# Performance work log

Hardware: AMD Instinct MI355X
Metric: run time of the kernel (lower is better)

Reference implementation:

```python
import jax, jax.numpy as jnp
import numpy as np

B, T, W, E, H, EMB, NVOCAB, WIN = 256, 200, 200, 768, 256, 32, 201, 8


def setup_inputs() -> dict:
    key = jax.random.key(0)
    ks = jax.random.split(key, 12)
    s = 0.05
    inputs = jax.random.normal(ks[0], (B, T, E), jnp.float32)
    full_word_embeddings = jax.random.normal(ks[1], (B, W, E), jnp.float32)
    lengths = jax.random.randint(ks[2], (B,), T // 2, T + 1)
    fix = jax.random.randint(ks[3], (B, T), 1, NVOCAB)
    fix_seq = jnp.where(jnp.arange(T)[None, :] < lengths[:, None], fix, 0)
    emb_table = (jax.random.normal(ks[4], (NVOCAB, EMB)) * s).at[0].set(0.0)  # padding_idx=0
    W_ih = jax.random.normal(ks[5], (3 * H, E + EMB)) * s  # torch GRU layout, gates r,z,n
    W_hh = jax.random.normal(ks[6], (3 * H, H)) * s
    b_ih = jax.random.normal(ks[7], (3 * H,)) * s
    b_hh = jax.random.normal(ks[8], (3 * H,)) * s
    W_out = jax.random.normal(ks[9], (E, H)) * s  # output_layer: Linear(H, E)
    b_out = jnp.zeros((E,), jnp.float32)
    W_dur = jax.random.normal(ks[10], (1, H)) * s  # duration_layer: Linear(H, 1)
    b_dur = jnp.zeros((1,), jnp.float32)
    return {"inputs": inputs, "fix_seq": fix_seq, "full_word_embeddings": full_word_embeddings,
            "lengths": lengths, "expert_id": 0, "emb_table": emb_table,
            "W_ih": W_ih, "b_ih": b_ih, "W_hh": W_hh, "b_hh": b_hh,
            "W_out": W_out, "b_out": b_out, "W_dur": W_dur, "b_dur": b_dur}


def _gru(x, W_ih, b_ih, W_hh, b_hh, h_dim):
    # x: [B,T,I]. Precompute input projections once, scan over time.
    xg = jnp.einsum('bti,gi->btg', x, W_ih) + b_ih  # [B,T,3H]

    def step(h, xg_t):
        hg = h @ W_hh.T + b_hh
        xr, xz, xn = jnp.split(xg_t, 3, axis=-1)
        hr, hz, hn = jnp.split(hg, 3, axis=-1)
        r = jax.nn.sigmoid(xr + hr)
        z = jax.nn.sigmoid(xz + hz)
        n = jnp.tanh(xn + r * hn)
        h_new = (1.0 - z) * n + z * h
        return h_new, h_new

    h0 = jnp.zeros((x.shape[0], h_dim), x.dtype)
    _, outs = jax.lax.scan(step, h0, jnp.swapaxes(xg, 0, 1))
    return jnp.swapaxes(outs, 0, 1)  # [B,T,H]


def reference(inputs, fix_seq, full_word_embeddings, lengths, expert_id,
              emb_table, W_ih, b_ih, W_hh, b_hh, W_out, b_out, W_dur, b_dur):
    del expert_id  # weights of the selected expert are passed directly
    valid_mask = fix_seq != 0
    scan_emb = emb_table[fix_seq]  # [B,T,32]
    rnn_in = jnp.concatenate([inputs, scan_emb], axis=-1)
    outputs = _gru(rnn_in, W_ih, b_ih, W_hh, b_hh, W_hh.shape[1])  # [B,T,H]
    # pad_packed_sequence zeros outputs beyond each sequence length
    tmask = jnp.arange(outputs.shape[1])[None, :] < lengths[:, None]
    outputs = outputs * tmask[..., None].astype(outputs.dtype)
    # dot attention: proj then scores against word embeddings
    proj = outputs @ W_out.T + b_out  # [B,T,E]
    logits = jnp.einsum('bte,bwe->btw', proj, full_word_embeddings)
    # saccade window mask around current fixation position
    wpos = jnp.arange(full_word_embeddings.shape[1])[None, None, :]
    dist = jnp.abs(wpos - fix_seq[..., None])
    sacc = (dist <= WIN) & valid_mask[..., None]
    logits = jnp.where(sacc, logits, -1e9)
    word_mask = jnp.sum(jnp.abs(full_word_embeddings), axis=-1) != 0
    logits = jnp.where(word_mask[:, None, :], logits, -1e9)
    dur_pred = (outputs @ W_dur.T + b_dur)[..., 0]  # [B,T]
    return logits, dur_pred
```

## Files before the change

kernel.cpp:

```cpp
#include <hip/hip_runtime.h>
#include <hip/hip_bf16.h>

typedef __attribute__((ext_vector_type(8))) short bf16x8;
typedef __attribute__((ext_vector_type(4))) float f32x4;
typedef __attribute__((ext_vector_type(4))) int   i32x4;

#define NB 256
#define NT 200
#define NW 200
#define NE 768
#define NH 256
#define NEMB 32
#define KIN 800
#define G3H 768
#define MROWS 51200

__device__ __forceinline__ float bf2f(unsigned short h) {
    return __uint_as_float(((unsigned)h) << 16);
}
__device__ __forceinline__ unsigned short f2bf(float f) {
    unsigned u = __float_as_uint(f);
    u += 0x7fff + ((u >> 16) & 1);
    return (unsigned short)(u >> 16);
}
__device__ __forceinline__ float sigm(float x) { return 1.0f / (1.0f + __expf(-x)); }
__device__ __forceinline__ float tanh_fast(float x) {
    float e = __expf(2.0f * x);
    return 1.0f - 2.0f / (e + 1.0f);
}

#if __has_builtin(__builtin_amdgcn_sdot4)
__device__ __forceinline__ int SDOT4(int a, int b, int c) {
    return __builtin_amdgcn_sdot4(a, b, c, false);
}
#else
__device__ __forceinline__ int SDOT4(int a, int b, int c) {
    #pragma unroll
    for (int j = 0; j < 4; j++)
        c += (int)(signed char)(a >> (8 * j)) * (int)(signed char)(b >> (8 * j));
    return c;
}
#endif

__device__ __forceinline__ void gload16(const void* g, void* l) {
    __builtin_amdgcn_global_load_lds((const __attribute__((address_space(1))) unsigned int*)g,
                                     (__attribute__((address_space(3))) unsigned int*)l,
                                     16, 0, 0);
}

__global__ void prep1(const float* __restrict__ inputs, const int* __restrict__ fix_seq,
                      const float* __restrict__ emb, const float* __restrict__ Wih,
                      const float* __restrict__ Wout, const float* __restrict__ bih,
                      const float* __restrict__ bhh,
                      unsigned short* __restrict__ Abf, unsigned short* __restrict__ Wihbf,
                      unsigned short* __restrict__ WoutTbf, float* __restrict__ biasC) {
    const long gid0 = (long)blockIdx.x * blockDim.x + threadIdx.x;
    if (gid0 < G3H) biasC[gid0] = bih[gid0] + (gid0 < 512 ? bhh[gid0] : 0.0f);
    const long NA = (long)MROWS * 100;
    const long NWU = 768L * 100;
    const long NOU = 256L * 96;
    const long total = NA + NWU + NOU;
    for (long u = gid0; u < total; u += (long)gridDim.x * blockDim.x) {
        bf16x8 v;
        unsigned short* dst;
        if (u < NA) {
            long row = u / 100;
            int c8 = (int)(u % 100) * 8;
            const float* s;
            if (c8 < NE) {
                s = inputs + row * NE + c8;
            } else {
                int fx = fix_seq[row];
                s = emb + (long)fx * NEMB + (c8 - NE);
            }
            #pragma unroll
            for (int j = 0; j < 8; j++) v[j] = (short)f2bf(s[j]);
            dst = Abf + row * KIN + c8;
        } else if (u < NA + NWU) {
            long u2 = u - NA;
            long row = u2 / 100;
            int c8 = (int)(u2 % 100) * 8;
            const float* s = Wih + row * KIN + c8;
            #pragma unroll
            for (int j = 0; j < 8; j++) v[j] = (short)f2bf(s[j]);
            dst = Wihbf + row * KIN + c8;
        } else {
            long u3 = u - NA - NWU;
            long row = u3 / 96;
            int c8 = (int)(u3 % 96) * 8;
            #pragma unroll
            for (int j = 0; j < 8; j++)
                v[j] = (short)f2bf(Wout[(long)(c8 + j) * NH + row]);
            dst = WoutTbf + row * NE + c8;
        }
        *(bf16x8*)dst = v;
    }
}

__global__ __launch_bounds__(256)
void gemm_bt128(const unsigned short* __restrict__ A,
                const unsigned short* __restrict__ Bw,
                const float* __restrict__ bias,
                unsigned short* __restrict__ Out,
                int M, int N, int K) {
    __shared__ unsigned short As[2][128 * 32];
    __shared__ unsigned short Bs[2][128 * 32];
    const int bid = (int)((blockIdx.x & 7) * (gridDim.x >> 3) + (blockIdx.x >> 3));
    const int nblk = N >> 7;
    const int m0 = (bid / nblk) << 7;
    const int n0 = (bid % nblk) << 7;
    const int tid = threadIdx.x;
    const int lane = tid & 63;
    const int wave = tid >> 6;
    const int wm = (wave >> 1) << 6;
    const int wn = (wave & 1) << 6;
    const int nk = K >> 5;

    const int srow = tid >> 2;
    const int sseg = (tid & 3) << 4;
    const char* gA0 = (const char*)(A + (long)(m0 + srow) * K) + sseg;
    const char* gA1 = (const char*)(A + (long)(m0 + 64 + srow) * K) + sseg;
    const char* gB0 = (const char*)(Bw + (long)(n0 + srow) * K) + sseg;
    const char* gB1 = (const char*)(Bw + (long)(n0 + 64 + srow) * K) + sseg;
    const int lofs = wave * 1024;

    f32x4 acc[4][4] = {};

    gload16(gA0, (char*)As[0] + lofs);
    gload16(gA1, (char*)As[0] + 4096 + lofs);
    gload16(gB0, (char*)Bs[0] + lofs);
    gload16(gB1, (char*)Bs[0] + 4096 + lofs);

    int cur = 0;
    for (int kt = 0; kt < nk; kt++) {
        if (kt + 1 < nk) {
            gload16(gA0 + (kt + 1) * 64, (char*)As[cur ^ 1] + lofs);
            gload16(gA1 + (kt + 1) * 64, (char*)As[cur ^ 1] + 4096 + lofs);
            gload16(gB0 + (kt + 1) * 64, (char*)Bs[cur ^ 1] + lofs);
            gload16(gB1 + (kt + 1) * 64, (char*)Bs[cur ^ 1] + 4096 + lofs);
            asm volatile("s_waitcnt vmcnt(4)" ::: "memory");
        } else {
            asm volatile("s_waitcnt vmcnt(0)" ::: "memory");
        }
        __builtin_amdgcn_sched_barrier(0);
        __builtin_amdgcn_s_barrier();
        __builtin_amdgcn_sched_barrier(0);
        bf16x8 af[4], bfr[4];
        #pragma unroll
        for (int mi = 0; mi < 4; mi++)
            af[mi] = *(const bf16x8*)((const char*)As[cur] +
                        (wm + mi * 16 + (lane & 15)) * 64 + ((lane >> 4) << 4));
        #pragma unroll
        for (int ni = 0; ni < 4; ni++)
            bfr[ni] = *(const bf16x8*)((const char*)Bs[cur] +
                        (wn + ni * 16 + (lane & 15)) * 64 + ((lane >> 4) << 4));
        #pragma unroll
        for (int mi = 0; mi < 4; mi++)
            #pragma unroll
            for (int ni = 0; ni < 4; ni++)
                acc[mi][ni] = __builtin_amdgcn_mfma_f32_16x16x32_bf16(
                                  af[mi], bfr[ni], acc[mi][ni], 0, 0, 0);
        asm volatile("s_waitcnt lgkmcnt(0)" ::: "memory");
        __builtin_amdgcn_sched_barrier(0);
        __builtin_amdgcn_s_barrier();
        __builtin_amdgcn_sched_barrier(0);
        cur ^= 1;
    }
    #pragma unroll
    for (int ni = 0; ni < 4; ni++) {
        const int col = n0 + wn + ni * 16 + (lane & 15);
        const float bv = bias[col];
        #pragma unroll
        for (int mi = 0; mi < 4; mi++) {
            const int row = m0 + wm + mi * 16 + ((lane >> 4) << 2);
            #pragma unroll
            for (int r = 0; r < 4; r++)
                Out[(long)(row + r) * N + col] = f2bf(acc[mi][ni][r] + bv);
        }
    }
}

__global__ __launch_bounds__(512)
void gemmG_f32(const float* __restrict__ fwe,
               const unsigned short* __restrict__ BwT,
               const float* __restrict__ bout,
               unsigned short* __restrict__ G,
               unsigned char* __restrict__ wmask,
               float* __restrict__ dvec) {
    __shared__ unsigned short As[128 * 32];
    __shared__ unsigned short Bs[256 * 32];
    __shared__ float Bo[G3H];
    const int m0 = (int)blockIdx.x << 7;
    const int tid = threadIdx.x;
    const int lane = tid & 63;
    const int wave = tid >> 6;
    const int wm = (wave >> 2) << 6;
    const int wn = (wave & 3) << 6;

    const int arow = tid >> 2;
    const int akq = tid & 3;
    const float* aptr = fwe + (long)(m0 + arow) * NE + akq * 8;
    char* la = (char*)As + arow * 64 + akq * 16;

    const int sseg = (tid & 3) << 4;
    const char* gBa = (const char*)(BwT + (long)arow * NE) + sseg;
    const char* gBb = (const char*)(BwT + (long)(128 + arow) * NE) + sseg;
    char* lBa = (char*)Bs + wave * 1024;
    char* lBb = (char*)Bs + 8192 + wave * 1024;

    for (int i = tid; i < G3H; i += 512) Bo[i] = bout[i];

    float4 fa0 = *(const float4*)(aptr);
    float4 fa1 = *(const float4*)(aptr + 4);

    f32x4 acc[4][4] = {};
    float asum = 0.0f, vdot = 0.0f;

    __syncthreads();

    for (int kt = 0; kt < 24; kt++) {
        __syncthreads();
        gload16(gBa + kt * 64, lBa);
        gload16(gBb + kt * 64, lBb);
        const float* bo = Bo + kt * 32 + akq * 8;
        const float4 b0 = *(const float4*)(bo);
        const float4 b1 = *(const float4*)(bo + 4);
        asum += fabsf(fa0.x) + fabsf(fa0.y) + fabsf(fa0.z) + fabsf(fa0.w)
              + fabsf(fa1.x) + fabsf(fa1.y) + fabsf(fa1.z) + fabsf(fa1.w);
        vdot += fa0.x * b0.x + fa0.y * b0.y + fa0.z * b0.z + fa0.w * b0.w
              + fa1.x * b1.x + fa1.y * b1.y + fa1.z * b1.z + fa1.w * b1.w;
        bf16x8 v;
        v[0] = (short)f2bf(fa0.x); v[1] = (short)f2bf(fa0.y);
        v[2] = (short)f2bf(fa0.z); v[3] = (short)f2bf(fa0.w);
        v[4] = (short)f2bf(fa1.x); v[5] = (short)f2bf(fa1.y);
        v[6] = (short)f2bf(fa1.z); v[7] = (short)f2bf(fa1.w);
        *(bf16x8*)la = v;
        asm volatile("s_waitcnt vmcnt(0)" ::: "memory");
        __syncthreads();
        if (kt + 1 < 24) {
            const float* ap = aptr + (kt + 1) * 32;
            fa0 = *(const float4*)(ap);
            fa1 = *(const float4*)(ap + 4);
        }
        bf16x8 af[4], bfr[4];
        #pragma unroll
        for (int mi = 0; mi < 4; mi++)
            af[mi] = *(const bf16x8*)((const char*)As +
                        (wm + mi * 16 + (lane & 15)) * 64 + ((lane >> 4) << 4));
        #pragma unroll
        for (int ni = 0; ni < 4; ni++)
            bfr[ni] = *(const bf16x8*)((const char*)Bs +
                        (wn + ni * 16 + (lane & 15)) * 64 + ((lane >> 4) << 4));
        #pragma unroll
        for (int mi = 0; mi < 4; mi++)
            #pragma unroll
            for (int ni = 0; ni < 4; ni++)
                acc[mi][ni] = __builtin_amdgcn_mfma_f32_16x16x32_bf16(
                                  af[mi], bfr[ni], acc[mi][ni], 0, 0, 0);
    }
    asum += __shfl_xor(asum, 1);  asum += __shfl_xor(asum, 2);
    vdot += __shfl_xor(vdot, 1);  vdot += __shfl_xor(vdot, 2);
    if (akq == 0) {
        wmask[m0 + arow] = (asum != 0.0f) ? 1 : 0;
        dvec[m0 + arow] = vdot;
    }
    #pragma unroll
    for (int ni = 0; ni < 4; ni++) {
        const int col = wn + ni * 16 + (lane & 15);
        #pragma unroll
        for (int mi = 0; mi < 4; mi++) {
            const int row = m0 + wm + mi * 16 + ((lane >> 4) << 2);
            #pragma unroll
            for (int r = 0; r < 4; r++)
                G[(long)(row + r) * NH + col] = f2bf(acc[mi][ni][r]);
        }
    }
}

__global__ __launch_bounds__(512, 2)
__attribute__((amdgpu_waves_per_eu(2, 2)))
void gru_scan(const unsigned short* __restrict__ xg,
              const float* __restrict__ Whh,
              const float* __restrict__ bhh,
              const int* __restrict__ lengths,
              unsigned short* __restrict__ hout) {
    __shared__ __align__(16) unsigned char h8[2][256];
    const int tid = threadIdx.x;
    const int lane = tid & 63;
    const int wave = tid >> 6;
    const int b = blockIdx.x;
    const int col = wave * 32 + (lane & 31);
    const int kh = lane >> 5;

    int W[3][32];
    #pragma unroll
    for (int g = 0; g < 3; g++) {
        const float* wr = Whh + (long)(g * 256 + col) * NH + kh * 128;
        #pragma unroll
        for (int d = 0; d < 32; d++) {
            const float4 f = *(const float4*)(wr + d * 4);
            unsigned pack = 0;
            #pragma unroll
            for (int j = 0; j < 4; j++) {
                const float fv = j == 0 ? f.x : j == 1 ? f.y : j == 2 ? f.z : f.w;
                int wq = (int)rintf(fv * 400.0f);
                wq = wq > 127 ? 127 : (wq < -127 ? -127 : wq);
                pack |= ((unsigned)(wq & 0xff)) << (8 * j);
            }
            W[g][d] = (int)pack;
        }
    }
    const float bhn = bhh[512 + col];
    const int len = lengths[b];
    if (tid < 128) ((unsigned*)h8)[tid] = 0u;

    const unsigned short* xrow = xg + (long)b * NT * G3H;
    unsigned short xv0 = xrow[col], xv1 = xrow[256 + col], xv2 = xrow[512 + col];
    float hp = 0.0f;
    const float ISC = 1.0f / (400.0f * 127.0f);
    const bool wlo = (lane < 32);

    asm volatile("s_waitcnt lgkmcnt(0)" ::: "memory");
    __builtin_amdgcn_sched_barrier(0);
    __builtin_amdgcn_s_barrier();
    __builtin_amdgcn_sched_barrier(0);

    for (int t = 0; t < NT; t++) {
        const unsigned char* hb = h8[(t + 1) & 1] + kh * 128;
        int p0a = 0, p0b = 0, p1a = 0, p1b = 0, p2a = 0, p2b = 0;
        #pragma unroll
        for (int r = 0; r < 8; r++) {
            const i32x4 hv = *(const i32x4*)(hb + r * 16);
            p0a = SDOT4(hv[0], W[0][r * 4 + 0], p0a);
            p1a = SDOT4(hv[0], W[1][r * 4 + 0], p1a);
            p2a = SDOT4(hv[0], W[2][r * 4 + 0], p2a);
            p0b = SDOT4(hv[1], W[0][r * 4 + 1], p0b);
            p1b = SDOT4(hv[1], W[1][r * 4 + 1], p1b);
            p2b = SDOT4(hv[1], W[2][r * 4 + 1], p2b);
            p0a = SDOT4(hv[2], W[0][r * 4 + 2], p0a);
            p1a = SDOT4(hv[2], W[1][r * 4 + 2], p1a);
            p2a = SDOT4(hv[2], W[2][r * 4 + 2], p2a);
            p0b = SDOT4(hv[3], W[0][r * 4 + 3], p0b);
            p1b = SDOT4(hv[3], W[1][r * 4 + 3], p1b);
            p2b = SDOT4(hv[3], W[2][r * 4 + 3], p2b);
        }
        int p0 = p0a + p0b, p1 = p1a + p1b, p2 = p2a + p2b;
        p0 += __shfl_xor(p0, 32);
        p1 += __shfl_xor(p1, 32);
        p2 += __shfl_xor(p2, 32);
        const float r = sigm(bf2f(xv0) + (float)p0 * ISC);
        const float z = sigm(bf2f(xv1) + (float)p1 * ISC);
        const float n = tanh_fast(bf2f(xv2) + r * ((float)p2 * ISC + bhn));
        hp = (1.0f - z) * n + z * hp;
        if (wlo) {
            h8[t & 1][col] = (unsigned char)((int)rintf(hp * 127.0f) & 0xff);
            hout[((long)b * NT + t) * NH + col] = (t < len) ? f2bf(hp) : (unsigned short)0;
        }
        if (t + 1 < NT) {
            const unsigned short* xn = xrow + (long)(t + 1) * G3H;
            xv0 = xn[col]; xv1 = xn[256 + col]; xv2 = xn[512 + col];
        }
        asm volatile("s_waitcnt lgkmcnt(0)" ::: "memory");
        __builtin_amdgcn_sched_barrier(0);
        __builtin_amdgcn_s_barrier();
        __builtin_amdgcn_sched_barrier(0);
    }
}

__global__ __launch_bounds__(256)
void logits_dur(const unsigned short* __restrict__ Hrow,
                const unsigned short* __restrict__ G,
                const int* __restrict__ fix_seq,
                const unsigned char* __restrict__ wmask,
                const float* __restrict__ dvec,
                const float* __restrict__ Wdur, const float* __restrict__ bdur,
                float* __restrict__ out) {
    __shared__ float dots[4][20];
    const int wv = threadIdx.x >> 6;
    const int gwave = (int)blockIdx.x * 4 + wv;
    const int lane = threadIdx.x & 63;
    const int l16 = lane & 15;
    const int grp = lane >> 4;
    const int b = gwave / NT;

    const unsigned short* hp = Hrow + (long)gwave * NH + l16 * 16;
    const bf16x8 h0 = *(const bf16x8*)hp;
    const bf16x8 h1 = *(const bf16x8*)(hp + 8);
    float hf[16];
    #pragma unroll
    for (int j = 0; j < 8; j++) { hf[j] = bf2f((unsigned short)h0[j]);
                                  hf[8 + j] = bf2f((unsigned short)h1[j]); }

    const int fix = fix_seq[gwave];
    const int wbase = fix - 8;

    if (fix != 0) {
        #pragma unroll
        for (int it = 0; it < 5; it++) {
            const int wi = it * 4 + grp;
            int w = wbase + wi;
            w = w < 0 ? 0 : (w > NW - 1 ? NW - 1 : w);
            const unsigned short* gp = G + ((long)b * NW + w) * NH + l16 * 16;
            const bf16x8 g0 = *(const bf16x8*)gp;
            const bf16x8 g1 = *(const bf16x8*)(gp + 8);
            float p = 0.0f;
            #pragma unroll
            for (int j = 0; j < 8; j++) {
                p += hf[j] * bf2f((unsigned short)g0[j]);
                p += hf[8 + j] * bf2f((unsigned short)g1[j]);
            }
            p += __shfl_xor(p, 1); p += __shfl_xor(p, 2);
            p += __shfl_xor(p, 4); p += __shfl_xor(p, 8);
            if (l16 == 0 && wi < 17) dots[wv][wi] = p;
        }
    }
    float pd = 0.0f;
    #pragma unroll
    for (int j = 0; j < 16; j++) pd += hf[j] * Wdur[l16 * 16 + j];
    pd += __shfl_xor(pd, 1); pd += __shfl_xor(pd, 2);
    pd += __shfl_xor(pd, 4); pd += __shfl_xor(pd, 8);
    if (lane == 0) out[(long)NB * NT * NW + gwave] = pd + bdur[0];

    __syncthreads();

    if (lane < 50) {
        float4 o;
        #pragma unroll
        for (int c = 0; c < 4; c++) {
            const int w = lane * 4 + c;
            const int wi = w - wbase;
            const int wic = wi < 0 ? 0 : (wi > 16 ? 16 : wi);
            const bool ok = (fix != 0) && ((unsigned)wi < 17u) && (wmask[b * NW + w] != 0);
            const float val = dots[wv][wic] + dvec[b * NW + w];
            ((float*)&o)[c] = ok ? val : -1e9f;
        }
        *(float4*)(out + (long)gwave * NW + lane * 4) = o;
    }
}

extern "C" void kernel_launch(void* const* d_in, const int* in_sizes, int n_in,
                              void* d_out, int out_size, void* d_ws, size_t ws_size,
                              hipStream_t stream) {
    (void)in_sizes; (void)n_in; (void)out_size; (void)ws_size;
    const float* inputs  = (const float*)d_in[0];
    const int*   fix_seq = (const int*)d_in[1];
    const float* fwe     = (const float*)d_in[2];
    const int*   lengths = (const int*)d_in[3];
    const float* emb     = (const float*)d_in[5];
    const float* Wih     = (const float*)d_in[6];
    const float* bih     = (const float*)d_in[7];
    const float* Whh     = (const float*)d_in[8];
    const float* bhh     = (const float*)d_in[9];
    const float* Wout    = (const float*)d_in[10];
    const float* bout    = (const float*)d_in[11];
    const float* Wdur    = (const float*)d_in[12];
    const float* bdur    = (const float*)d_in[13];
    float* out = (float*)d_out;

    char* ws = (char*)d_ws;
    unsigned short* Abf     = (unsigned short*)(ws);
    unsigned short* xgbf    = (unsigned short*)(ws + 81920000);
    unsigned short* hout    = (unsigned short*)(ws + 160563200);
    unsigned short* Wihbf   = (unsigned short*)(ws + 186777600);
    unsigned short* WoutTbf = (unsigned short*)(ws + 188006400);
    unsigned char*  wmask   = (unsigned char*)(ws + 188399616);
    float*          biasC   = (float*)(ws + 188450816);
    float*          dvec    = (float*)(ws + 188453888);
    unsigned short* Gbf     = Abf;

    prep1<<<2048, 256, 0, stream>>>(inputs, fix_seq, emb, Wih, Wout, bih, bhh,
                                    Abf, Wihbf, WoutTbf, biasC);
    gemm_bt128<<<400 * 6, 256, 0, stream>>>(Abf, Wihbf, biasC, xgbf, MROWS, G3H, KIN);
    gemmG_f32<<<400, 512, 0, stream>>>(fwe, WoutTbf, bout, Gbf, wmask, dvec);
    gru_scan<<<256, 512, 0, stream>>>(xgbf, Whh, bhh, lengths, hout);
    logits_dur<<<12800, 256, 0, stream>>>(hout, Gbf, fix_seq, wmask, dvec, Wdur, bdur, out);
}
```

Before: 463.4 us.

## Widen input-projection GEMM tile to 128x256 with 8 waves; pow2 prep indexing

The input-projection GEMM moves from 128x128 tiles with 4 waves to 128x256 tiles with 8 waves. Each A tile is now reused across twice as many output columns, which halves the number of blocks and the global traffic for A. The prep kernel replaces divide and modulo by 100 or 96 with power-of-two shift indexing and skips the padding lanes, removing integer divisions in exchange for some idle iterations. The epilogue, which is not shown, must still match the new wave layout; the larger LDS footprint may also lower occupancy.

```diff
diff --git a/kernel.cpp b/kernel.cpp
--- a/kernel.cpp
+++ b/kernel.cpp
@@ -56,16 +56,18 @@
                       unsigned short* __restrict__ WoutTbf, float* __restrict__ biasC) {
     const long gid0 = (long)blockIdx.x * blockDim.x + threadIdx.x;
     if (gid0 < G3H) biasC[gid0] = bih[gid0] + (gid0 < 512 ? bhh[gid0] : 0.0f);
-    const long NA = (long)MROWS * 100;
-    const long NWU = 768L * 100;
-    const long NOU = 256L * 96;
+    const long NA = (long)MROWS << 7;
+    const long NWU = 768L << 7;
+    const long NOU = 256L << 7;
     const long total = NA + NWU + NOU;
     for (long u = gid0; u < total; u += (long)gridDim.x * blockDim.x) {
         bf16x8 v;
         unsigned short* dst;
         if (u < NA) {
-            long row = u / 100;
-            int c8 = (int)(u % 100) * 8;
+            const long row = u >> 7;
+            const int c = (int)(u & 127);
+            if (c >= 100) continue;
+            const int c8 = c << 3;
             const float* s;
             if (c8 < NE) {
                 s = inputs + row * NE + c8;
@@ -77,17 +79,21 @@
             for (int j = 0; j < 8; j++) v[j] = (short)f2bf(s[j]);
             dst = Abf + row * KIN + c8;
         } else if (u < NA + NWU) {
-            long u2 = u - NA;
-            long row = u2 / 100;
-            int c8 = (int)(u2 % 100) * 8;
+            const long u2 = u - NA;
+            const long row = u2 >> 7;
+            const int c = (int)(u2 & 127);
+            if (c >= 100) continue;
+            const int c8 = c << 3;
             const float* s = Wih + row * KIN + c8;
             #pragma unroll
             for (int j = 0; j < 8; j++) v[j] = (short)f2bf(s[j]);
             dst = Wihbf + row * KIN + c8;
         } else {
-            long u3 = u - NA - NWU;
-            long row = u3 / 96;
-            int c8 = (int)(u3 % 96) * 8;
+            const long u3 = u - NA - NWU;
+            const long row = u3 >> 7;
+            const int c = (int)(u3 & 127);
+            if (c >= 96) continue;
+            const int c8 = c << 3;
             #pragma unroll
             for (int j = 0; j < 8; j++)
                 v[j] = (short)f2bf(Wout[(long)(c8 + j) * NH + row]);
@@ -97,48 +103,45 @@
     }
 }
 
-__global__ __launch_bounds__(256)
+__global__ __launch_bounds__(512, 4)
 void gemm_bt128(const unsigned short* __restrict__ A,
                 const unsigned short* __restrict__ Bw,
                 const float* __restrict__ bias,
                 unsigned short* __restrict__ Out,
                 int M, int N, int K) {
     __shared__ unsigned short As[2][128 * 32];
-    __shared__ unsigned short Bs[2][128 * 32];
+    __shared__ unsigned short Bs[2][256 * 32];
     const int bid = (int)((blockIdx.x & 7) * (gridDim.x >> 3) + (blockIdx.x >> 3));
-    const int nblk = N >> 7;
+    const int nblk = N >> 8;
     const int m0 = (bid / nblk) << 7;
-    const int n0 = (bid % nblk) << 7;
+    const int n0 = (bid % nblk) << 8;
     const int tid = threadIdx.x;
     const int lane = tid & 63;
     const int wave = tid >> 6;
-    const int wm = (wave >> 1) << 6;
-    const int wn = (wave & 1) << 6;
+    const int wm = (wave >> 2) << 6;
+    const int wn = (wave & 3) << 6;
     const int nk = K >> 5;
 
     const int srow = tid >> 2;
     const int sseg = (tid & 3) << 4;
-    const char* gA0 = (const char*)(A + (long)(m0 + srow) * K) + sseg;
-    const char* gA1 = (const char*)(A + (long)(m0 + 64 + srow) * K) + sseg;
+    const char* gA  = (const char*)(A + (long)(m0 + srow) * K) + sseg;
     const char* gB0 = (const char*)(Bw + (long)(n0 + srow) * K) + sseg;
-    const char* gB1 = (const char*)(Bw + (long)(n0 + 64 + srow) * K) + sseg;
+    const char* gB1 = (const char*)(Bw + (long)(n0 + 128 + srow) * K) + sseg;
     const int lofs = wave * 1024;
 
     f32x4 acc[4][4] = {};
 
-    gload16(gA0, (char*)As[0] + lofs);
-    gload16(gA1, (char*)As[0] + 4096 + lofs);
+    gload16(gA,  (char*)As[0] + lofs);
     gload16(gB0, (char*)Bs[0] + lofs);
-    gload16(gB1, (char*)Bs[0] + 4096 + lofs);
+    gload16(gB1, (char*)Bs[0] + 8192 + lofs);
 
     int cur = 0;
     for (int kt = 0; kt < nk; kt++) {
         if (kt + 1 < nk) {
-            gload16(gA0 + (kt + 1) * 64, (char*)As[cur ^ 1] + lofs);
-            gload16(gA1 + (kt + 1) * 64, (char*)As[cur ^ 1] + 4096 + lofs);
+            gload16(gA  + (kt + 1) * 64, (char*)As[cur ^ 1] + lofs);
             gload16(gB0 + (kt + 1) * 64, (char*)Bs[cur ^ 1] + lofs);
-            gload16(gB1 + (kt + 1) * 64, (char*)Bs[cur ^ 1] + 4096 + lofs);
-            asm volatile("s_waitcnt vmcnt(4)" ::: "memory");
+            gload16(gB1 + (kt + 1) * 64, (char*)Bs[cur ^ 1] + 8192 + lofs);
+            asm volatile("s_waitcnt vmcnt(3)" ::: "memory");
         } else {
             asm volatile("s_waitcnt vmcnt(0)" ::: "memory");
         }
@@ -470,7 +473,7 @@
 
     prep1<<<2048, 256, 0, stream>>>(inputs, fix_seq, emb, Wih, Wout, bih, bhh,
                                     Abf, Wihbf, WoutTbf, biasC);
-    gemm_bt128<<<400 * 6, 256, 0, stream>>>(Abf, Wihbf, biasC, xgbf, MROWS, G3H, KIN);
+    gemm_bt128<<<400 * 3, 512, 0, stream>>>(Abf, Wihbf, biasC, xgbf, MROWS, G3H, KIN);
     gemmG_f32<<<400, 512, 0, stream>>>(fwe, WoutTbf, bout, Gbf, wmask, dvec);
     gru_scan<<<256, 512, 0, stream>>>(xgbf, Whh, bhh, lengths, hout);
     logits_dur<<<12800, 256, 0, stream>>>(hout, Gbf, fix_seq, wmask, dvec, Wdur, bdur, out);
```

Measured after the change: 461.3 us. About the same (-0.5%).
